# Performance work log

Measured on AMD Instinct MI355X. Metric: run time of the kernel, lower is better.

The kernel has to match this reference:

```python
import jax, jax.numpy as jnp
import numpy as np

C_IN = 768
CA = 384


def dwconv3d(x, w, b, pad):
    # x: [B, Ca, T, H, W], w: [Ca, 1, kd, kh, kw] depthwise (groups=Ca)
    y = jax.lax.conv_general_dilated(
        x, w, window_strides=(1, 1, 1), padding=pad,
        dimension_numbers=("NCDHW", "OIDHW", "NCDHW"),
        feature_group_count=w.shape[0])
    return y + b[None, :, None, None, None]


def setup_inputs() -> dict:
    key = jax.random.key(0)
    ks = jax.random.split(key, 9)
    s = 0.02
    inp = {
        "x": jax.random.normal(ks[0], (128, 197, C_IN), dtype=jnp.float32),
        # main branch params (torch Linear weight transposed to [in, out])
        "w1": jax.random.normal(ks[1], (C_IN, CA), dtype=jnp.float32) * s,
        "b1": jnp.zeros((CA,), jnp.float32),
        "cw": jax.random.normal(ks[2], (CA, 1, 3, 3, 3), dtype=jnp.float32) * s,
        "cb": jnp.zeros((CA,), jnp.float32),
        "w2": jax.random.normal(ks[3], (CA, C_IN), dtype=jnp.float32) * s,
        "b2": jnp.zeros((C_IN,), jnp.float32),
        # offset-adapter params (depthwise kernel (1,3,3))
        "ow1": jax.random.normal(ks[4], (C_IN, CA), dtype=jnp.float32) * s,
        "ob1": jnp.zeros((CA,), jnp.float32),
        "ocw": jax.random.normal(ks[5], (CA, 1, 1, 3, 3), dtype=jnp.float32) * s,
        "ocb": jnp.zeros((CA,), jnp.float32),
        "ow2": jax.random.normal(ks[6], (CA, C_IN), dtype=jnp.float32) * s,
        "ob2": jnp.zeros((C_IN,), jnp.float32),
        "T": 8,
    }
    return inp


def reference(x, w1, b1, cw, cb, w2, b2, ow1, ob1, ocw, ocb, ow2, ob2, T):
    BT, L, C = x.shape
    B = BT // T
    H = W = int(round((L - 1) ** 0.5))
    Ca = w1.shape[1]

    xs = x[:, 1:, :].reshape(B, T, H * W, C)  # drop CLS token

    # ---- OffsetAdapter branch ----
    x_former = jnp.concatenate([xs[:, :1], xs[:, :-1]], axis=1)  # former_id = [0,0,1,...,T-2]
    off = xs - x_former
    off = off @ ow1 + ob1                                   # [B,T,HW,Ca]
    off = off.reshape(B, T, H, W, Ca).transpose(0, 4, 1, 2, 3)  # [B,Ca,T,H,W]
    off = dwconv3d(off, ocw, ocb, [(0, 0), (1, 1), (1, 1)])
    off = off.transpose(0, 2, 3, 4, 1).reshape(BT, H * W, Ca)
    off = off @ ow2 + ob2                                   # [BT,HW,C]

    # ---- main branch ----
    y = xs @ w1 + b1                                        # [B,T,HW,Ca]
    y = y.reshape(B, T, H, W, Ca).transpose(0, 4, 1, 2, 3)  # [B,Ca,T,H,W]
    y = dwconv3d(y, cw, cb, [(1, 1), (1, 1), (1, 1)])
    y = y.transpose(0, 2, 3, 4, 1).reshape(BT, H * W, Ca)
    y = y @ w2 + b2 + off                                   # [BT,HW,C]

    # residual add into patch tokens (CLS passthrough)
    return x.at[:, 1:, :].add(y)
```

## Files before the change

kernel.cpp:

```cpp
#include <hip/hip_runtime.h>

#define Cc   768
#define CAc  384
#define Bc   16
#define Tc   8
#define Hc   14
#define Wc   14
#define HWc  196
#define Lc   197
#define BTc  128
#define Mc   25088

typedef unsigned short u16;
typedef __attribute__((ext_vector_type(4))) float f32x4;
typedef __attribute__((ext_vector_type(4))) short s16x4;
typedef __attribute__((ext_vector_type(8))) short s16x8;

__device__ __forceinline__ u16 f2b(float f) {
  union { float f; unsigned u; } v; v.f = f;
  unsigned r = (v.u + 0x7FFFu + ((v.u >> 16) & 1u)) >> 16;
  return (u16)r;
}
__device__ __forceinline__ float b2f(u16 h) {
  union { unsigned u; float f; } v; v.u = ((unsigned)h) << 16;
  return v.f;
}

__global__ void wt_kernel(const float* __restrict__ w, u16* __restrict__ wT, int K, int N) {
  int idx = blockIdx.x * 256 + threadIdx.x;
  if (idx >= K * N) return;
  int n = idx / K, k = idx - n * K;
  wT[idx] = f2b(w[k * N + n]);
}

__global__ void cwt_kernel(const float* __restrict__ cw, float* __restrict__ cwT, int taps) {
  int idx = blockIdx.x * 256 + threadIdx.x;
  if (idx >= taps * CAc) return;
  int t = idx / CAc, c = idx - t * CAc;
  cwT[idx] = cw[c * taps + t];
}

__global__ void prep_kernel(const float* __restrict__ x, u16* __restrict__ xb, u16* __restrict__ db) {
  int idx = blockIdx.x * 256 + threadIdx.x;
  if (idx >= Mc * 96) return;
  int r = idx / 96;
  int cg = idx - r * 96;
  int b = r / (Tc * HWc);
  int rem = r - b * (Tc * HWc);
  int t = rem / HWc;
  int hw = rem - t * HWc;
  long xoff = ((long)(b * Tc + t) * Lc + 1 + hw) * Cc + cg * 8;
  long poff = (t > 0) ? (xoff - (long)Lc * Cc) : xoff;
  f32x4 ca = *(const f32x4*)(x + xoff);
  f32x4 cb = *(const f32x4*)(x + xoff + 4);
  f32x4 pa = *(const f32x4*)(x + poff);
  f32x4 pb = *(const f32x4*)(x + poff + 4);
  s16x8 xo, dd;
  #pragma unroll
  for (int q = 0; q < 4; ++q) {
    xo[q]     = (short)f2b(ca[q]);
    xo[q + 4] = (short)f2b(cb[q]);
    dd[q]     = (short)f2b(ca[q] - pa[q]);
    dd[q + 4] = (short)f2b(cb[q] - pb[q]);
  }
  *(s16x8*)(xb + (long)r * Cc + cg * 8) = xo;
  *(s16x8*)(db + (long)r * Cc + cg * 8) = dd;
}

__global__ void cls_kernel(const float* __restrict__ x, float* __restrict__ out) {
  int idx = blockIdx.x * 256 + threadIdx.x;
  if (idx >= BTc * (Cc / 4)) return;
  int bt = idx / (Cc / 4);
  int c4 = (idx - bt * (Cc / 4)) * 4;
  long o = (long)bt * Lc * Cc + c4;
  *(f32x4*)(out + o) = *(const f32x4*)(x + o);
}

#define SP 68

__global__ __launch_bounds__(256, 2) void gemm1_kernel(
    const u16* __restrict__ xb, const u16* __restrict__ db,
    const u16* __restrict__ w1T, const u16* __restrict__ ow1T,
    const float* __restrict__ b1v, const float* __restrict__ ob1v,
    u16* __restrict__ y1, u16* __restrict__ o1)
{
  __shared__ u16 lA[128 * SP];
  __shared__ u16 lB[128 * SP];
  const u16* A    = blockIdx.z ? db   : xb;
  const u16* Wt   = blockIdx.z ? ow1T : w1T;
  const float* bv = blockIdx.z ? ob1v : b1v;
  u16* outp       = blockIdx.z ? o1   : y1;

  int tid = threadIdx.x;
  int m0 = blockIdx.x * 128;
  int n0 = blockIdx.y * 128;
  int wave = tid >> 6, lane = tid & 63;
  int wm = (wave >> 1) * 64, wn = (wave & 1) * 64;
  int lrow = lane & 15, lgrp = lane >> 4;
  int srow = tid >> 3;
  int scol = (tid & 7) * 8;

  f32x4 acc[4][4];
  #pragma unroll
  for (int i = 0; i < 4; ++i)
    #pragma unroll
    for (int j = 0; j < 4; ++j) acc[i][j] = (f32x4){0.f, 0.f, 0.f, 0.f};

  for (int kt = 0; kt < 12; ++kt) {
    int k0 = kt * 64;
    #pragma unroll
    for (int p = 0; p < 4; ++p) {
      int r = p * 32 + srow;
      s16x8 va = *(const s16x8*)(A  + (long)(m0 + r) * Cc + k0 + scol);
      s16x8 vb = *(const s16x8*)(Wt + (long)(n0 + r) * Cc + k0 + scol);
      *(s16x4*)(lA + r * SP + scol)     = ((s16x4*)&va)[0];
      *(s16x4*)(lA + r * SP + scol + 4) = ((s16x4*)&va)[1];
      *(s16x4*)(lB + r * SP + scol)     = ((s16x4*)&vb)[0];
      *(s16x4*)(lB + r * SP + scol + 4) = ((s16x4*)&vb)[1];
    }
    __syncthreads();
    #pragma unroll
    for (int kk = 0; kk < 4; ++kk) {
      s16x4 af[4], bf[4];
      #pragma unroll
      for (int i = 0; i < 4; ++i) af[i] = *(const s16x4*)(lA + (wm + i * 16 + lrow) * SP + kk * 16 + lgrp * 4);
      #pragma unroll
      for (int j = 0; j < 4; ++j) bf[j] = *(const s16x4*)(lB + (wn + j * 16 + lrow) * SP + kk * 16 + lgrp * 4);
      #pragma unroll
      for (int i = 0; i < 4; ++i)
        #pragma unroll
        for (int j = 0; j < 4; ++j)
          acc[i][j] = __builtin_amdgcn_mfma_f32_16x16x16bf16_1k(af[i], bf[j], acc[i][j], 0, 0, 0);
    }
    __syncthreads();
  }
  #pragma unroll
  for (int i = 0; i < 4; ++i) {
    #pragma unroll
    for (int j = 0; j < 4; ++j) {
      int n = n0 + wn + j * 16 + lrow;
      float bb = bv[n];
      #pragma unroll
      for (int q = 0; q < 4; ++q) {
        int m = m0 + wm + i * 16 + lgrp * 4 + q;
        outp[(long)m * CAc + n] = f2b(acc[i][j][q] + bb);
      }
    }
  }
}

__global__ __launch_bounds__(256, 2) void gemm2_kernel(
    const u16* __restrict__ c1, const u16* __restrict__ c2,
    const u16* __restrict__ w2T, const u16* __restrict__ ow2T,
    const float* __restrict__ b2v, const float* __restrict__ ob2v,
    const float* __restrict__ x, float* __restrict__ out)
{
  __shared__ u16 lA[128 * SP];
  __shared__ u16 lB[128 * SP];
  int tid = threadIdx.x;
  int m0 = blockIdx.x * 128;
  int n0 = blockIdx.y * 128;
  int wave = tid >> 6, lane = tid & 63;
  int wm = (wave >> 1) * 64, wn = (wave & 1) * 64;
  int lrow = lane & 15, lgrp = lane >> 4;
  int srow = tid >> 3;
  int scol = (tid & 7) * 8;

  f32x4 acc[4][4];
  #pragma unroll
  for (int i = 0; i < 4; ++i)
    #pragma unroll
    for (int j = 0; j < 4; ++j) acc[i][j] = (f32x4){0.f, 0.f, 0.f, 0.f};

  for (int kt = 0; kt < 12; ++kt) {
    int half = kt >= 6;
    const u16* Ap = half ? c2 : c1;
    const u16* Wp = half ? ow2T : w2T;
    int k0 = (half ? (kt - 6) : kt) * 64;
    #pragma unroll
    for (int p = 0; p < 4; ++p) {
      int r = p * 32 + srow;
      s16x8 va = *(const s16x8*)(Ap + (long)(m0 + r) * CAc + k0 + scol);
      s16x8 vb = *(const s16x8*)(Wp + (long)(n0 + r) * CAc + k0 + scol);
      *(s16x4*)(lA + r * SP + scol)     = ((s16x4*)&va)[0];
      *(s16x4*)(lA + r * SP + scol + 4) = ((s16x4*)&va)[1];
      *(s16x4*)(lB + r * SP + scol)     = ((s16x4*)&vb)[0];
      *(s16x4*)(lB + r * SP + scol + 4) = ((s16x4*)&vb)[1];
    }
    __syncthreads();
    #pragma unroll
    for (int kk = 0; kk < 4; ++kk) {
      s16x4 af[4], bf[4];
      #pragma unroll
      for (int i = 0; i < 4; ++i) af[i] = *(const s16x4*)(lA + (wm + i * 16 + lrow) * SP + kk * 16 + lgrp * 4);
      #pragma unroll
      for (int j = 0; j < 4; ++j) bf[j] = *(const s16x4*)(lB + (wn + j * 16 + lrow) * SP + kk * 16 + lgrp * 4);
      #pragma unroll
      for (int i = 0; i < 4; ++i)
        #pragma unroll
        for (int j = 0; j < 4; ++j)
          acc[i][j] = __builtin_amdgcn_mfma_f32_16x16x16bf16_1k(af[i], bf[j], acc[i][j], 0, 0, 0);
    }
    __syncthreads();
  }
  #pragma unroll
  for (int i = 0; i < 4; ++i) {
    #pragma unroll
    for (int q = 0; q < 4; ++q) {
      int m = m0 + wm + i * 16 + lgrp * 4 + q;
      int bt = m / HWc;
      int hw = m - bt * HWc;
      long base = ((long)bt * Lc + 1 + hw) * Cc;
      #pragma unroll
      for (int j = 0; j < 4; ++j) {
        int n = n0 + wn + j * 16 + lrow;
        out[base + n] = x[base + n] + acc[i][j][q] + b2v[n] + ob2v[n];
      }
    }
  }
}

__global__ void conv_kernel(const u16* __restrict__ in, const float* __restrict__ wT,
                            const float* __restrict__ bias, u16* __restrict__ outp,
                            int is3d)
{
  int bth = blockIdx.x;
  int h = bth % Hc;
  int bt = bth / Hc;
  int t = bt % Tc;
  int tid = threadIdx.x;
  int dtlo = is3d ? -1 : 0, dthi = is3d ? 1 : 0;
  for (int it = tid; it < Wc * 48; it += 256) {
    int wq = it / 48;
    int c = (it - wq * 48) * 8;
    float a[8] = {0.f, 0.f, 0.f, 0.f, 0.f, 0.f, 0.f, 0.f};
    int tap = 0;
    for (int dt = dtlo; dt <= dthi; ++dt) {
      int tt = t + dt;
      bool tok = (tt >= 0) && (tt < Tc);
      for (int dh = -1; dh <= 1; ++dh) {
        int hh = h + dh;
        bool hok = (hh >= 0) && (hh < Hc);
        for (int dw = -1; dw <= 1; ++dw, ++tap) {
          int ww = wq + dw;
          if (!tok || !hok || ww < 0 || ww >= Wc) continue;
          const u16* ip = in + ((long)(bt + dt) * HWc + hh * Wc + ww) * CAc + c;
          s16x8 v = *(const s16x8*)ip;
          const float* wp = wT + tap * CAc + c;
          f32x4 w0 = *(const f32x4*)wp;
          f32x4 w1 = *(const f32x4*)(wp + 4);
          #pragma unroll
          for (int q = 0; q < 4; ++q) {
            a[q]     += b2f((u16)v[q])     * w0[q];
            a[q + 4] += b2f((u16)v[q + 4]) * w1[q];
          }
        }
      }
    }
    s16x8 o;
    #pragma unroll
    for (int q = 0; q < 8; ++q) o[q] = (short)f2b(a[q] + bias[c + q]);
    *(s16x8*)(outp + ((long)bt * HWc + h * Wc + wq) * CAc + c) = o;
  }
}

extern "C" void kernel_launch(void* const* d_in, const int* in_sizes, int n_in,
                              void* d_out, int out_size, void* d_ws, size_t ws_size,
                              hipStream_t stream) {
  const float* x   = (const float*)d_in[0];
  const float* w1  = (const float*)d_in[1];
  const float* b1  = (const float*)d_in[2];
  const float* cw  = (const float*)d_in[3];
  const float* cb  = (const float*)d_in[4];
  const float* w2  = (const float*)d_in[5];
  const float* b2  = (const float*)d_in[6];
  const float* ow1 = (const float*)d_in[7];
  const float* ob1 = (const float*)d_in[8];
  const float* ocw = (const float*)d_in[9];
  const float* ocb = (const float*)d_in[10];
  const float* ow2 = (const float*)d_in[11];
  const float* ob2 = (const float*)d_in[12];
  float* out = (float*)d_out;
  char* ws = (char*)d_ws;

  u16*  w1T  = (u16*) (ws + 0);
  u16*  ow1T = (u16*) (ws + 589824);
  u16*  w2T  = (u16*) (ws + 1179648);
  u16*  ow2T = (u16*) (ws + 1769472);
  float* cwT = (float*)(ws + 2359296);
  float* ocwT= (float*)(ws + 2400768);
  u16*  xb   = (u16*) (ws + 2414592);
  u16*  db   = (u16*) (ws + 40949760);
  u16*  y1   = (u16*) (ws + 79484928);
  u16*  o1   = (u16*) (ws + 98752512);
  u16*  c1   = (u16*) (ws + 2414592);
  u16*  c2   = (u16*) (ws + 2414592 + 19267584);

  wt_kernel<<<1152, 256, 0, stream>>>(w1, w1T, 768, 384);
  wt_kernel<<<1152, 256, 0, stream>>>(ow1, ow1T, 768, 384);
  wt_kernel<<<1152, 256, 0, stream>>>(w2, w2T, 384, 768);
  wt_kernel<<<1152, 256, 0, stream>>>(ow2, ow2T, 384, 768);
  cwt_kernel<<<41, 256, 0, stream>>>(cw, cwT, 27);
  cwt_kernel<<<14, 256, 0, stream>>>(ocw, ocwT, 9);
  prep_kernel<<<9408, 256, 0, stream>>>(x, xb, db);
  cls_kernel<<<96, 256, 0, stream>>>(x, out);
  gemm1_kernel<<<dim3(196, 3, 2), 256, 0, stream>>>(xb, db, w1T, ow1T, b1, ob1, y1, o1);
  conv_kernel<<<1792, 256, 0, stream>>>(y1, cwT, cb, c1, 1);
  conv_kernel<<<1792, 256, 0, stream>>>(o1, ocwT, ocb, c2, 0);
  gemm2_kernel<<<dim3(196, 6, 1), 256, 0, stream>>>(c1, c2, w2T, ow2T, b2, ob2, x, out);
}
```

Baseline: 372.1 us.

## Fuse bf16 prep into gemm1, compute both branches per block, use 16x16x32 MFMA

The separate prep kernel is removed. gemm1 now reads fp32 x directly, forms the bf16 token and temporal-difference tiles in-kernel, and computes both the main and offset GEMMs in one block, which has four LDS tiles and two accumulator sets. Both GEMMs switch to the 16x16x32 bf16 MFMA with 128-bit LDS accesses, and the LDS row pitch changes to 72. The two conv launches are merged into one grid, removing the xb/db round trip through memory. In exchange, gemm1 launches half as many blocks, and the doubled LDS and accumulator registers may lower occupancy.

```diff
diff --git a/kernel.cpp b/kernel.cpp
--- a/kernel.cpp
+++ b/kernel.cpp
@@ -2,7 +2,6 @@
 
 #define Cc   768
 #define CAc  384
-#define Bc   16
 #define Tc   8
 #define Hc   14
 #define Wc   14
@@ -40,33 +39,6 @@
   cwT[idx] = cw[c * taps + t];
 }
 
-__global__ void prep_kernel(const float* __restrict__ x, u16* __restrict__ xb, u16* __restrict__ db) {
-  int idx = blockIdx.x * 256 + threadIdx.x;
-  if (idx >= Mc * 96) return;
-  int r = idx / 96;
-  int cg = idx - r * 96;
-  int b = r / (Tc * HWc);
-  int rem = r - b * (Tc * HWc);
-  int t = rem / HWc;
-  int hw = rem - t * HWc;
-  long xoff = ((long)(b * Tc + t) * Lc + 1 + hw) * Cc + cg * 8;
-  long poff = (t > 0) ? (xoff - (long)Lc * Cc) : xoff;
-  f32x4 ca = *(const f32x4*)(x + xoff);
-  f32x4 cb = *(const f32x4*)(x + xoff + 4);
-  f32x4 pa = *(const f32x4*)(x + poff);
-  f32x4 pb = *(const f32x4*)(x + poff + 4);
-  s16x8 xo, dd;
-  #pragma unroll
-  for (int q = 0; q < 4; ++q) {
-    xo[q]     = (short)f2b(ca[q]);
-    xo[q + 4] = (short)f2b(cb[q]);
-    dd[q]     = (short)f2b(ca[q] - pa[q]);
-    dd[q + 4] = (short)f2b(cb[q] - pb[q]);
-  }
-  *(s16x8*)(xb + (long)r * Cc + cg * 8) = xo;
-  *(s16x8*)(db + (long)r * Cc + cg * 8) = dd;
-}
-
 __global__ void cls_kernel(const float* __restrict__ x, float* __restrict__ out) {
   int idx = blockIdx.x * 256 + threadIdx.x;
   if (idx >= BTc * (Cc / 4)) return;
@@ -76,20 +48,19 @@
   *(f32x4*)(out + o) = *(const f32x4*)(x + o);
 }
 
-#define SP 68
+#define SP 72
 
 __global__ __launch_bounds__(256, 2) void gemm1_kernel(
-    const u16* __restrict__ xb, const u16* __restrict__ db,
+    const float* __restrict__ x,
     const u16* __restrict__ w1T, const u16* __restrict__ ow1T,
     const float* __restrict__ b1v, const float* __restrict__ ob1v,
     u16* __restrict__ y1, u16* __restrict__ o1)
 {
-  __shared__ u16 lA[128 * SP];
-  __shared__ u16 lB[128 * SP];
-  const u16* A    = blockIdx.z ? db   : xb;
-  const u16* Wt   = blockIdx.z ? ow1T : w1T;
-  const float* bv = blockIdx.z ? ob1v : b1v;
-  u16* outp       = blockIdx.z ? o1   : y1;
+  __shared__ u16 lds[4 * 128 * SP];
+  u16* lXS = lds;
+  u16* lDF = lds + 128 * SP;
+  u16* lW  = lds + 2 * 128 * SP;
+  u16* lOW = lds + 3 * 128 * SP;
 
   int tid = threadIdx.x;
   int m0 = blockIdx.x * 128;
@@ -100,37 +71,66 @@
   int srow = tid >> 3;
   int scol = (tid & 7) * 8;
 
-  f32x4 acc[4][4];
+  f32x4 am[4][4], ao[4][4];
   #pragma unroll
   for (int i = 0; i < 4; ++i)
     #pragma unroll
-    for (int j = 0; j < 4; ++j) acc[i][j] = (f32x4){0.f, 0.f, 0.f, 0.f};
+    for (int j = 0; j < 4; ++j) { am[i][j] = (f32x4){0,0,0,0}; ao[i][j] = (f32x4){0,0,0,0}; }
 
   for (int kt = 0; kt < 12; ++kt) {
     int k0 = kt * 64;
     #pragma unroll
     for (int p = 0; p < 4; ++p) {
       int r = p * 32 + srow;
-      s16x8 va = *(const s16x8*)(A  + (long)(m0 + r) * Cc + k0 + scol);
-      s16x8 vb = *(const s16x8*)(Wt + (long)(n0 + r) * Cc + k0 + scol);
-      *(s16x4*)(lA + r * SP + scol)     = ((s16x4*)&va)[0];
-      *(s16x4*)(lA + r * SP + scol + 4) = ((s16x4*)&va)[1];
-      *(s16x4*)(lB + r * SP + scol)     = ((s16x4*)&vb)[0];
-      *(s16x4*)(lB + r * SP + scol + 4) = ((s16x4*)&vb)[1];
+      int gm = m0 + r;
+      int bt = gm / HWc;
+      int hw = gm - bt * HWc;
+      int t = bt & 7;
+      long xoff = ((long)bt * Lc + 1 + hw) * Cc + k0 + scol;
+      long poff = (t > 0) ? (xoff - (long)Lc * Cc) : xoff;
+      f32x4 ca = *(const f32x4*)(x + xoff);
+      f32x4 cb = *(const f32x4*)(x + xoff + 4);
+      f32x4 pa = *(const f32x4*)(x + poff);
+      f32x4 pb = *(const f32x4*)(x + poff + 4);
+      s16x8 xo, dd;
+      #pragma unroll
+      for (int q = 0; q < 4; ++q) {
+        xo[q]     = (short)f2b(ca[q]);
+        xo[q + 4] = (short)f2b(cb[q]);
+        dd[q]     = (short)f2b(ca[q] - pa[q]);
+        dd[q + 4] = (short)f2b(cb[q] - pb[q]);
+      }
+      int wr = n0 + r;
+      s16x8 vw = *(const s16x8*)(w1T  + (long)wr * Cc + k0 + scol);
+      s16x8 vo = *(const s16x8*)(ow1T + (long)wr * Cc + k0 + scol);
+      *(s16x8*)(lXS + r * SP + scol) = xo;
+      *(s16x8*)(lDF + r * SP + scol) = dd;
+      *(s16x8*)(lW  + r * SP + scol) = vw;
+      *(s16x8*)(lOW + r * SP + scol) = vo;
     }
     __syncthreads();
     #pragma unroll
-    for (int kk = 0; kk < 4; ++kk) {
-      s16x4 af[4], bf[4];
-      #pragma unroll
-      for (int i = 0; i < 4; ++i) af[i] = *(const s16x4*)(lA + (wm + i * 16 + lrow) * SP + kk * 16 + lgrp * 4);
-      #pragma unroll
-      for (int j = 0; j < 4; ++j) bf[j] = *(const s16x4*)(lB + (wn + j * 16 + lrow) * SP + kk * 16 + lgrp * 4);
+    for (int kk = 0; kk < 2; ++kk) {
+      s16x8 ax[4], ad[4], bw[4], bo[4];
+      #pragma unroll
+      for (int i = 0; i < 4; ++i) {
+        int ro = (wm + i * 16 + lrow) * SP + kk * 32 + lgrp * 8;
+        ax[i] = *(const s16x8*)(lXS + ro);
+        ad[i] = *(const s16x8*)(lDF + ro);
+      }
+      #pragma unroll
+      for (int j = 0; j < 4; ++j) {
+        int ro = (wn + j * 16 + lrow) * SP + kk * 32 + lgrp * 8;
+        bw[j] = *(const s16x8*)(lW + ro);
+        bo[j] = *(const s16x8*)(lOW + ro);
+      }
       #pragma unroll
       for (int i = 0; i < 4; ++i)
         #pragma unroll
-        for (int j = 0; j < 4; ++j)
-          acc[i][j] = __builtin_amdgcn_mfma_f32_16x16x16bf16_1k(af[i], bf[j], acc[i][j], 0, 0, 0);
+        for (int j = 0; j < 4; ++j) {
+          am[i][j] = __builtin_amdgcn_mfma_f32_16x16x32_bf16(ax[i], bw[j], am[i][j], 0, 0, 0);
+          ao[i][j] = __builtin_amdgcn_mfma_f32_16x16x32_bf16(ad[i], bo[j], ao[i][j], 0, 0, 0);
+        }
     }
     __syncthreads();
   }
@@ -139,11 +139,12 @@
     #pragma unroll
     for (int j = 0; j < 4; ++j) {
       int n = n0 + wn + j * 16 + lrow;
-      float bb = bv[n];
+      float bb = b1v[n], ob = ob1v[n];
       #pragma unroll
       for (int q = 0; q < 4; ++q) {
         int m = m0 + wm + i * 16 + lgrp * 4 + q;
-        outp[(long)m * CAc + n] = f2b(acc[i][j][q] + bb);
+        y1[(long)m * CAc + n] = f2b(am[i][j][q] + bb);
+        o1[(long)m * CAc + n] = f2b(ao[i][j][q] + ob);
       }
     }
   }
@@ -170,7 +171,7 @@
   #pragma unroll
   for (int i = 0; i < 4; ++i)
     #pragma unroll
-    for (int j = 0; j < 4; ++j) acc[i][j] = (f32x4){0.f, 0.f, 0.f, 0.f};
+    for (int j = 0; j < 4; ++j) acc[i][j] = (f32x4){0,0,0,0};
 
   for (int kt = 0; kt < 12; ++kt) {
     int half = kt >= 6;
@@ -182,24 +183,22 @@
       int r = p * 32 + srow;
       s16x8 va = *(const s16x8*)(Ap + (long)(m0 + r) * CAc + k0 + scol);
       s16x8 vb = *(const s16x8*)(Wp + (long)(n0 + r) * CAc + k0 + scol);
-      *(s16x4*)(lA + r * SP + scol)     = ((s16x4*)&va)[0];
-      *(s16x4*)(lA + r * SP + scol + 4) = ((s16x4*)&va)[1];
-      *(s16x4*)(lB + r * SP + scol)     = ((s16x4*)&vb)[0];
-      *(s16x4*)(lB + r * SP + scol + 4) = ((s16x4*)&vb)[1];
+      *(s16x8*)(lA + r * SP + scol) = va;
+      *(s16x8*)(lB + r * SP + scol) = vb;
     }
     __syncthreads();
     #pragma unroll
-    for (int kk = 0; kk < 4; ++kk) {
-      s16x4 af[4], bf[4];
-      #pragma unroll
-      for (int i = 0; i < 4; ++i) af[i] = *(const s16x4*)(lA + (wm + i * 16 + lrow) * SP + kk * 16 + lgrp * 4);
-      #pragma unroll
-      for (int j = 0; j < 4; ++j) bf[j] = *(const s16x4*)(lB + (wn + j * 16 + lrow) * SP + kk * 16 + lgrp * 4);
+    for (int kk = 0; kk < 2; ++kk) {
+      s16x8 af[4], bf[4];
+      #pragma unroll
+      for (int i = 0; i < 4; ++i) af[i] = *(const s16x8*)(lA + (wm + i * 16 + lrow) * SP + kk * 32 + lgrp * 8);
+      #pragma unroll
+      for (int j = 0; j < 4; ++j) bf[j] = *(const s16x8*)(lB + (wn + j * 16 + lrow) * SP + kk * 32 + lgrp * 8);
       #pragma unroll
       for (int i = 0; i < 4; ++i)
         #pragma unroll
         for (int j = 0; j < 4; ++j)
-          acc[i][j] = __builtin_amdgcn_mfma_f32_16x16x16bf16_1k(af[i], bf[j], acc[i][j], 0, 0, 0);
+          acc[i][j] = __builtin_amdgcn_mfma_f32_16x16x32_bf16(af[i], bf[j], acc[i][j], 0, 0, 0);
     }
     __syncthreads();
   }
@@ -220,10 +219,17 @@
   }
 }
 
-__global__ void conv_kernel(const u16* __restrict__ in, const float* __restrict__ wT,
-                            const float* __restrict__ bias, u16* __restrict__ outp,
-                            int is3d)
+__global__ void conv_kernel(const u16* __restrict__ in1, const float* __restrict__ wT1,
+                            const float* __restrict__ bias1, u16* __restrict__ out1,
+                            const u16* __restrict__ in2, const float* __restrict__ wT2,
+                            const float* __restrict__ bias2, u16* __restrict__ out2)
 {
+  int is3d = (blockIdx.y == 0);
+  const u16* in = is3d ? in1 : in2;
+  const float* wT = is3d ? wT1 : wT2;
+  const float* bias = is3d ? bias1 : bias2;
+  u16* outp = is3d ? out1 : out2;
+
   int bth = blockIdx.x;
   int h = bth % Hc;
   int bt = bth / Hc;
@@ -233,7 +239,7 @@
   for (int it = tid; it < Wc * 48; it += 256) {
     int wq = it / 48;
     int c = (it - wq * 48) * 8;
-    float a[8] = {0.f, 0.f, 0.f, 0.f, 0.f, 0.f, 0.f, 0.f};
+    float a[8] = {0,0,0,0,0,0,0,0};
     int tap = 0;
     for (int dt = dtlo; dt <= dthi; ++dt) {
       int tt = t + dt;
@@ -289,12 +295,10 @@
   u16*  ow2T = (u16*) (ws + 1769472);
   float* cwT = (float*)(ws + 2359296);
   float* ocwT= (float*)(ws + 2400768);
-  u16*  xb   = (u16*) (ws + 2414592);
-  u16*  db   = (u16*) (ws + 40949760);
-  u16*  y1   = (u16*) (ws + 79484928);
-  u16*  o1   = (u16*) (ws + 98752512);
-  u16*  c1   = (u16*) (ws + 2414592);
-  u16*  c2   = (u16*) (ws + 2414592 + 19267584);
+  u16*  y1   = (u16*) (ws + 2414592);
+  u16*  o1   = (u16*) (ws + 21682176);
+  u16*  c1   = (u16*) (ws + 40949760);
+  u16*  c2   = (u16*) (ws + 60217344);
 
   wt_kernel<<<1152, 256, 0, stream>>>(w1, w1T, 768, 384);
   wt_kernel<<<1152, 256, 0, stream>>>(ow1, ow1T, 768, 384);
@@ -302,10 +306,8 @@
   wt_kernel<<<1152, 256, 0, stream>>>(ow2, ow2T, 384, 768);
   cwt_kernel<<<41, 256, 0, stream>>>(cw, cwT, 27);
   cwt_kernel<<<14, 256, 0, stream>>>(ocw, ocwT, 9);
-  prep_kernel<<<9408, 256, 0, stream>>>(x, xb, db);
   cls_kernel<<<96, 256, 0, stream>>>(x, out);
-  gemm1_kernel<<<dim3(196, 3, 2), 256, 0, stream>>>(xb, db, w1T, ow1T, b1, ob1, y1, o1);
-  conv_kernel<<<1792, 256, 0, stream>>>(y1, cwT, cb, c1, 1);
-  conv_kernel<<<1792, 256, 0, stream>>>(o1, ocwT, ocb, c2, 0);
-  gemm2_kernel<<<dim3(196, 6, 1), 256, 0, stream>>>(c1, c2, w2T, ow2T, b2, ob2, x, out);
-}
+  gemm1_kernel<<<dim3(196, 3), 256, 0, stream>>>(x, w1T, ow1T, b1, ob1, y1, o1);
+  conv_kernel<<<dim3(1792, 2), 256, 0, stream>>>(y1, cwT, cb, c1, o1, ocwT, ocb, c2);
+  gemm2_kernel<<<dim3(196, 6), 256, 0, stream>>>(c1, c2, w2T, ow2T, b2, ob2, x, out);
+}
```

Measured after the change: 395.3 us. +6.2%, slower.
